# Kernel tuning notes

Hardware: AMD Instinct MI355X
Metric: run time of the kernel (lower is better)

## Reference

```python
import jax, jax.numpy as jnp
import numpy as np

LN_EPS = 1e-5


def setup_inputs() -> dict:
    key = jax.random.key(0)
    ks = jax.random.split(key, 8)
    N, H, E, D, B = 262144, 768, 768, 2048, 65536
    return {
        "u_t": jax.random.normal(ks[0], (B, E), dtype=jnp.float32),
        "s_i": jax.random.randint(ks[1], (B,), 0, N, dtype=jnp.int64),
        "speaker_embeddings": jax.random.normal(ks[2], (N, H), dtype=jnp.float32),
        "W1": jax.random.normal(ks[3], (D, H + E), dtype=jnp.float32) * 0.02,
        "b1": jax.random.normal(ks[4], (D,), dtype=jnp.float32) * 0.02,
        "W2": jax.random.normal(ks[5], (H, D), dtype=jnp.float32) * 0.02,
        "b2": jax.random.normal(ks[6], (H,), dtype=jnp.float32) * 0.02,
        "ln_gamma": jnp.ones((H,), dtype=jnp.float32),
        "ln_beta": jnp.zeros((H,), dtype=jnp.float32),
    }


def reference(u_t, s_i, speaker_embeddings, W1, b1, W2, b2, ln_gamma, ln_beta):
    # gather speaker vectors: [B, H]
    h_t = speaker_embeddings[s_i]
    # concat [u_t, h_t] along features: [B, E+H]
    x = jnp.concatenate([u_t, h_t], axis=-1)
    # Linear -> GELU (exact, torch default) -> (Dropout=identity in eval)
    h = jax.nn.gelu(jnp.einsum("bf,df->bd", x, W1) + b1, approximate=False)
    # Linear -> (Dropout=identity) : [B, H]
    y = jnp.einsum("bd,hd->bh", h, W2) + b2
    # LayerNorm over last dim
    mu = jnp.mean(y, axis=-1, keepdims=True)
    var = jnp.mean((y - mu) ** 2, axis=-1, keepdims=True)
    new_h_t = (y - mu) * jax.lax.rsqrt(var + LN_EPS) * ln_gamma + ln_beta
    # scatter-add back into the memory table (duplicates accumulate)
    updated = speaker_embeddings.at[s_i].add(new_h_t)
    return new_h_t, updated
```

## Files before the change

### kernel.cpp

```cpp
#include <hip/hip_runtime.h>
#include <hip/hip_bf16.h>

typedef unsigned short u16;
typedef unsigned int u32;
typedef short bf16x8 __attribute__((ext_vector_type(8)));
typedef float f32x4 __attribute__((ext_vector_type(4)));

#define BAR() asm volatile("s_barrier" ::: "memory")
#define WAITV8() asm volatile("s_waitcnt vmcnt(8)" ::: "memory")
#define WAITV4() asm volatile("s_waitcnt vmcnt(4)" ::: "memory")
#define WAITV0() asm volatile("s_waitcnt vmcnt(0)" ::: "memory")
#define WAITL() asm volatile("s_waitcnt lgkmcnt(0)" ::: "memory")

__device__ __forceinline__ unsigned pk2(float lo, float hi) {
    unsigned a = (unsigned)__builtin_bit_cast(u16, __float2bfloat16(lo));
    unsigned b = (unsigned)__builtin_bit_cast(u16, __float2bfloat16(hi));
    return a | (b << 16);
}
__device__ __forceinline__ u16 f2bf(float v) {
    return __builtin_bit_cast(u16, __float2bfloat16(v));
}
__device__ __forceinline__ void gl_lds16(const u16* g, u16* l) {
    __builtin_amdgcn_global_load_lds(
        (const __attribute__((address_space(1))) u32*)g,
        (__attribute__((address_space(3))) u32*)l, 16, 0, 0);
}

__global__ void cvtbf(const float4* __restrict__ s, uint2* __restrict__ d, int n4) {
    int i = blockIdx.x * blockDim.x + threadIdx.x;
    int stride = gridDim.x * blockDim.x;
    for (; i < n4; i += stride) {
        float4 f = s[i];
        uint2 o;
        o.x = pk2(f.x, f.y);
        o.y = pk2(f.z, f.w);
        d[i] = o;
    }
}

__global__ __launch_bounds__(256) void xbuild(const float* __restrict__ u_t,
                                              const float* __restrict__ emb,
                                              const int* __restrict__ s_i,
                                              u16* __restrict__ xb) {
    const long u = (long)blockIdx.x * blockDim.x + threadIdx.x;
    const int row = (int)(u / 192);
    const int c8 = (int)(u % 192);
    const float* src = (c8 < 96) ? (u_t + (long)row * 768 + c8 * 8)
                                 : (emb + (long)s_i[row] * 768 + (c8 - 96) * 8);
    float4 f0 = ((const float4*)src)[0];
    float4 f1 = ((const float4*)src)[1];
    uint4 o;
    o.x = pk2(f0.x, f0.y);
    o.y = pk2(f0.z, f0.w);
    o.z = pk2(f1.x, f1.y);
    o.w = pk2(f1.z, f1.w);
    *(uint4*)(xb + u * 8) = o;
}

template <int LDK, int NT, int TN, int EPI, int CMOD>
__global__ __launch_bounds__(512, 2) void gemm256(
    const u16* __restrict__ Ag, const u16* __restrict__ Bg,
    const float* __restrict__ bias, u16* __restrict__ outb,
    float* __restrict__ outf, const float4* __restrict__ csrc,
    float4* __restrict__ cdst, long ccount, int cstride) {
    __shared__ __align__(16) u16 lds[65536];

    const int tid = threadIdx.x;
    const int nblk = (int)gridDim.x;
    const int chunk = nblk >> 3;
    const int swz = ((int)blockIdx.x & 7) * chunk + ((int)blockIdx.x >> 3);

    if constexpr (CMOD > 0) {
        if ((swz % CMOD) == CMOD - 1) {
            long i = (long)(swz / CMOD) * 512 + tid;
            for (; i < ccount; i += cstride) cdst[i] = csrc[i];
            return;
        }
    }
    const int tile = (CMOD > 0) ? (swz - swz / CMOD) : swz;
    const int tm = tile / TN, tn = tile % TN;
    const long rowBase = (long)tm * 256;
    const long colBase = (long)tn * 256;

    const int lane = tid & 63;
    const int wv = tid >> 6;
    const int wm = wv >> 2;
    const int wn = wv & 3;

    const int srow = tid >> 2;
    const int gch = (tid & 3) ^ ((srow >> 1) & 3);
    const u16* pA = Ag + (rowBase + srow) * (long)LDK + gch * 8;
    const u16* pB = Bg + (colBase + srow) * (long)LDK + gch * 8;
    const int dstBase = wv * 512;

    auto stageA = [&](int kt, int b) {
        const u16* s = pA + kt * 32;
        u16* d = lds + b * 16384 + dstBase;
        gl_lds16(s, d);
        gl_lds16(s + (long)128 * LDK, d + 4096);
    };
    auto stageB = [&](int kt, int b) {
        const u16* s = pB + kt * 32;
        u16* d = lds + b * 16384 + 8192 + dstBase;
        gl_lds16(s, d);
        gl_lds16(s + (long)128 * LDK, d + 4096);
    };

    const int l15 = lane & 15, lc = lane >> 4;
    int offA[8], offB[4];
#pragma unroll
    for (int i = 0; i < 8; ++i) {
        int r = wm * 128 + i * 16 + l15;
        offA[i] = r * 32 + ((lc ^ ((r >> 1) & 3)) << 3);
    }
#pragma unroll
    for (int n = 0; n < 4; ++n) {
        int r = wn * 64 + n * 16 + l15;
        offB[n] = r * 32 + ((lc ^ ((r >> 1) & 3)) << 3);
    }

    f32x4 acc[8][4];
    const f32x4 zero = {0.f, 0.f, 0.f, 0.f};
#pragma unroll
    for (int m = 0; m < 8; ++m)
#pragma unroll
        for (int n = 0; n < 4; ++n) acc[m][n] = zero;

    stageA(0, 0); stageB(0, 0);
    stageA(1, 1); stageB(1, 1);
    stageA(2, 2); stageB(2, 2);
    WAITV8();
    BAR();

    bf16x8 bA[4], bB[4];
    for (int kt = 0; kt < NT; ++kt) {
        const int b = kt & 3;
        const u16* rA = lds + b * 16384;
        const u16* rB = rA + 8192;
        const bool pf = (kt + 3 < NT);

#pragma unroll
        for (int n = 0; n < 4; ++n) bB[n] = *(const bf16x8*)(rB + offB[n]);
#pragma unroll
        for (int m = 0; m < 4; ++m) bA[m] = *(const bf16x8*)(rA + offA[m]);
        if (pf) stageA(kt + 3, (kt + 3) & 3);
        BAR();
        WAITL();
        __builtin_amdgcn_s_setprio(1);
#pragma unroll
        for (int m = 0; m < 4; ++m)
#pragma unroll
            for (int n = 0; n < 4; ++n)
                acc[m][n] = __builtin_amdgcn_mfma_f32_16x16x32_bf16(bA[m], bB[n], acc[m][n], 0, 0, 0);
        __builtin_amdgcn_s_setprio(0);
        BAR();

#pragma unroll
        for (int m = 0; m < 4; ++m) bA[m] = *(const bf16x8*)(rA + offA[4 + m]);
        if (pf) stageB(kt + 3, (kt + 3) & 3);
        BAR();
        WAITL();
        __builtin_amdgcn_s_setprio(1);
#pragma unroll
        for (int m = 0; m < 4; ++m)
#pragma unroll
            for (int n = 0; n < 4; ++n)
                acc[4 + m][n] = __builtin_amdgcn_mfma_f32_16x16x32_bf16(bA[m], bB[n], acc[4 + m][n], 0, 0, 0);
        __builtin_amdgcn_s_setprio(0);
        if (pf) { WAITV8(); }
        else if (kt + 2 < NT) { WAITV4(); }
        else { WAITV0(); }
        BAR();
    }

    const int N = TN * 256;
#pragma unroll
    for (int n = 0; n < 4; ++n) {
        long gc = colBase + wn * 64 + n * 16 + l15;
        float bv = bias[gc];
#pragma unroll
        for (int i = 0; i < 8; ++i) {
            long gr = rowBase + wm * 128 + i * 16 + (lc << 2);
#pragma unroll
            for (int j = 0; j < 4; ++j) {
                float v = acc[i][n][j] + bv;
                if constexpr (EPI == 0) {
                    v = 0.5f * v * (1.0f + erff(v * 0.70710678118f));
                    outb[(gr + j) * N + gc] = f2bf(v);
                } else {
                    outf[(gr + j) * N + gc] = v;
                }
            }
        }
    }
}

__global__ __launch_bounds__(256) void ln_scatter(float* __restrict__ y,
                                                  const float* __restrict__ gamma,
                                                  const float* __restrict__ beta,
                                                  const int* __restrict__ s_i,
                                                  float* __restrict__ upd) {
    const int lane = threadIdx.x & 63;
    const long row = (long)blockIdx.x * 4 + (threadIdx.x >> 6);
    const long base = row * 768;
    float v[12];
#pragma unroll
    for (int i = 0; i < 12; ++i) v[i] = y[base + i * 64 + lane];
    float s = 0.f, q = 0.f;
#pragma unroll
    for (int i = 0; i < 12; ++i) { s += v[i]; q += v[i] * v[i]; }
#pragma unroll
    for (int off = 32; off > 0; off >>= 1) {
        s += __shfl_xor(s, off, 64);
        q += __shfl_xor(q, off, 64);
    }
    const float mu = s * (1.f / 768.f);
    const float var = q * (1.f / 768.f) - mu * mu;
    const float inv = rsqrtf(var + 1e-5f);
    const long si = s_i[row];
#pragma unroll
    for (int i = 0; i < 12; ++i) {
        int c = i * 64 + lane;
        float r = (v[i] - mu) * inv * gamma[c] + beta[c];
        y[base + c] = r;
        atomicAdd(&upd[si * 768 + c], r);
    }
}

__global__ void copy4(const float4* __restrict__ s, float4* __restrict__ d, long n) {
    long i = (long)blockIdx.x * blockDim.x + threadIdx.x;
    long stride = (long)gridDim.x * blockDim.x;
    for (; i < n; i += stride) d[i] = s[i];
}

extern "C" void kernel_launch(void* const* d_in, const int* in_sizes, int n_in,
                              void* d_out, int out_size, void* d_ws, size_t ws_size,
                              hipStream_t stream) {
    const float* u_t = (const float*)d_in[0];
    const int* s_i = (const int*)d_in[1];
    const float* emb = (const float*)d_in[2];
    const float* W1 = (const float*)d_in[3];
    const float* b1 = (const float*)d_in[4];
    const float* W2 = (const float*)d_in[5];
    const float* b2 = (const float*)d_in[6];
    const float* gamma = (const float*)d_in[7];
    const float* beta = (const float*)d_in[8];

    float* out = (float*)d_out;
    float* newh = out;
    float* upd = out + 50331648L;

    u16* base = (u16*)upd;
    u16* xb = base;
    u16* w1b = base + 100663296L;
    u16* hbuf = base + 103809024L;
    u16* w2b = base + 238026752L;

    const float4* embq = (const float4*)emb;
    float4* updq = (float4*)upd;

    cvtbf<<<1024, 256, 0, stream>>>((const float4*)W1, (uint2*)w1b, 786432);
    cvtbf<<<1024, 256, 0, stream>>>((const float4*)W2, (uint2*)w2b, 393216);
    xbuild<<<49152, 256, 0, stream>>>(u_t, emb, s_i, xb);
    gemm256<1536, 48, 8, 0, 5><<<2560, 512, 0, stream>>>(
        xb, w1b, b1, hbuf, nullptr,
        embq + 29949952L, updq + 29949952L, 20381696L, 262144);
    gemm256<2048, 64, 3, 1, 4><<<1024, 512, 0, stream>>>(
        hbuf, w2b, b2, nullptr, newh,
        embq, updq, 12976128L, 131072);
    copy4<<<2048, 256, 0, stream>>>(embq + 12976128L, updq + 12976128L, 16973824L);
    ln_scatter<<<16384, 256, 0, stream>>>(newh, gamma, beta, s_i, upd);
}
```

Measured before the change: 1.427 ms.

## Replace pipelined 256x256 GEMM with simple unpipelined 128x128 tile GEMM

Replaces the 512-thread 256x256-tile GEMM, which used a 4-stage global-to-LDS prefetch pipeline, split barriers, priority hints, and copy blocks interleaved with the embedding-table copy, with a 256-thread 128x128-tile kernel. The new kernel loads a single K=64 stage and synchronises twice per iteration, so nothing is prefetched. The embedding copy is moved entirely into a standalone copy kernel. This looks like a simplification or fallback that gives up latency hiding and reuse per tile in exchange for more blocks and simpler code.

```diff
diff --git a/kernel.cpp b/kernel.cpp
--- a/kernel.cpp
+++ b/kernel.cpp
@@ -5,12 +5,6 @@
 typedef unsigned int u32;
 typedef short bf16x8 __attribute__((ext_vector_type(8)));
 typedef float f32x4 __attribute__((ext_vector_type(4)));
-
-#define BAR() asm volatile("s_barrier" ::: "memory")
-#define WAITV8() asm volatile("s_waitcnt vmcnt(8)" ::: "memory")
-#define WAITV4() asm volatile("s_waitcnt vmcnt(4)" ::: "memory")
-#define WAITV0() asm volatile("s_waitcnt vmcnt(0)" ::: "memory")
-#define WAITL() asm volatile("s_waitcnt lgkmcnt(0)" ::: "memory")
 
 __device__ __forceinline__ unsigned pk2(float lo, float hi) {
     unsigned a = (unsigned)__builtin_bit_cast(u16, __float2bfloat16(lo));
@@ -57,133 +51,94 @@
     *(uint4*)(xb + u * 8) = o;
 }
 
-template <int LDK, int NT, int TN, int EPI, int CMOD>
-__global__ __launch_bounds__(512, 2) void gemm256(
+template <int LDK, int NT, int TN, int EPI>
+__global__ __launch_bounds__(256) void gemm128(
     const u16* __restrict__ Ag, const u16* __restrict__ Bg,
     const float* __restrict__ bias, u16* __restrict__ outb,
-    float* __restrict__ outf, const float4* __restrict__ csrc,
-    float4* __restrict__ cdst, long ccount, int cstride) {
-    __shared__ __align__(16) u16 lds[65536];
+    float* __restrict__ outf) {
+    __shared__ __align__(16) u16 As[8192];
+    __shared__ __align__(16) u16 Bs[8192];
 
     const int tid = threadIdx.x;
-    const int nblk = (int)gridDim.x;
-    const int chunk = nblk >> 3;
-    const int swz = ((int)blockIdx.x & 7) * chunk + ((int)blockIdx.x >> 3);
-
-    if constexpr (CMOD > 0) {
-        if ((swz % CMOD) == CMOD - 1) {
-            long i = (long)(swz / CMOD) * 512 + tid;
-            for (; i < ccount; i += cstride) cdst[i] = csrc[i];
-            return;
-        }
-    }
-    const int tile = (CMOD > 0) ? (swz - swz / CMOD) : swz;
+    const int lane = tid & 63;
+    const int cpx = (int)gridDim.x >> 3;
+    const int tile = ((int)blockIdx.x & 7) * cpx + ((int)blockIdx.x >> 3);
     const int tm = tile / TN, tn = tile % TN;
-    const long rowBase = (long)tm * 256;
-    const long colBase = (long)tn * 256;
-
-    const int lane = tid & 63;
+    const long rowBase = (long)tm * 128;
+    const long colBase = (long)tn * 128;
+
+    const int srow = tid >> 3;
+    const int sc = tid & 7;
+    const u16* gA[4];
+    const u16* gB[4];
+#pragma unroll
+    for (int p = 0; p < 4; ++p) {
+        int row = p * 32 + srow;
+        int gch = sc ^ (row & 7);
+        gA[p] = Ag + (rowBase + row) * (long)LDK + gch * 8;
+        gB[p] = Bg + (colBase + row) * (long)LDK + gch * 8;
+    }
+
+    auto stage = [&](int kt) {
+#pragma unroll
+        for (int p = 0; p < 4; ++p) {
+            gl_lds16(gA[p] + kt * 64, As + p * 2048 + tid * 8);
+            gl_lds16(gB[p] + kt * 64, Bs + p * 2048 + tid * 8);
+        }
+    };
+
+    const int l15 = lane & 15, lc = lane >> 4;
     const int wv = tid >> 6;
-    const int wm = wv >> 2;
-    const int wn = wv & 3;
-
-    const int srow = tid >> 2;
-    const int gch = (tid & 3) ^ ((srow >> 1) & 3);
-    const u16* pA = Ag + (rowBase + srow) * (long)LDK + gch * 8;
-    const u16* pB = Bg + (colBase + srow) * (long)LDK + gch * 8;
-    const int dstBase = wv * 512;
-
-    auto stageA = [&](int kt, int b) {
-        const u16* s = pA + kt * 32;
-        u16* d = lds + b * 16384 + dstBase;
-        gl_lds16(s, d);
-        gl_lds16(s + (long)128 * LDK, d + 4096);
-    };
-    auto stageB = [&](int kt, int b) {
-        const u16* s = pB + kt * 32;
-        u16* d = lds + b * 16384 + 8192 + dstBase;
-        gl_lds16(s, d);
-        gl_lds16(s + (long)128 * LDK, d + 4096);
-    };
-
-    const int l15 = lane & 15, lc = lane >> 4;
-    int offA[8], offB[4];
-#pragma unroll
-    for (int i = 0; i < 8; ++i) {
-        int r = wm * 128 + i * 16 + l15;
-        offA[i] = r * 32 + ((lc ^ ((r >> 1) & 3)) << 3);
-    }
+    const int wr = wv >> 1, wc = wv & 1;
+    int offA[2][4], offB[2][4];
+#pragma unroll
+    for (int kk = 0; kk < 2; ++kk) {
+#pragma unroll
+        for (int m = 0; m < 4; ++m) {
+            int r = wr * 64 + m * 16 + l15;
+            offA[kk][m] = r * 64 + ((((kk * 4 + lc)) ^ (r & 7)) << 3);
+            int c = wc * 64 + m * 16 + l15;
+            offB[kk][m] = c * 64 + ((((kk * 4 + lc)) ^ (c & 7)) << 3);
+        }
+    }
+
+    f32x4 acc[4][4];
+    const f32x4 zero = {0.f, 0.f, 0.f, 0.f};
+#pragma unroll
+    for (int m = 0; m < 4; ++m)
+#pragma unroll
+        for (int n = 0; n < 4; ++n) acc[m][n] = zero;
+
+    for (int kt = 0; kt < NT; ++kt) {
+        stage(kt);
+        __syncthreads();
+#pragma unroll
+        for (int kk = 0; kk < 2; ++kk) {
+            bf16x8 a[4], b[4];
+#pragma unroll
+            for (int m = 0; m < 4; ++m) a[m] = *(const bf16x8*)(As + offA[kk][m]);
+#pragma unroll
+            for (int n = 0; n < 4; ++n) b[n] = *(const bf16x8*)(Bs + offB[kk][n]);
+#pragma unroll
+            for (int m = 0; m < 4; ++m)
+#pragma unroll
+                for (int n = 0; n < 4; ++n)
+                    acc[m][n] = __builtin_amdgcn_mfma_f32_16x16x32_bf16(a[m], b[n], acc[m][n], 0, 0, 0);
+        }
+        __syncthreads();
+    }
+
+    const int N = TN * 128;
 #pragma unroll
     for (int n = 0; n < 4; ++n) {
-        int r = wn * 64 + n * 16 + l15;
-        offB[n] = r * 32 + ((lc ^ ((r >> 1) & 3)) << 3);
-    }
-
-    f32x4 acc[8][4];
-    const f32x4 zero = {0.f, 0.f, 0.f, 0.f};
-#pragma unroll
-    for (int m = 0; m < 8; ++m)
-#pragma unroll
-        for (int n = 0; n < 4; ++n) acc[m][n] = zero;
-
-    stageA(0, 0); stageB(0, 0);
-    stageA(1, 1); stageB(1, 1);
-    stageA(2, 2); stageB(2, 2);
-    WAITV8();
-    BAR();
-
-    bf16x8 bA[4], bB[4];
-    for (int kt = 0; kt < NT; ++kt) {
-        const int b = kt & 3;
-        const u16* rA = lds + b * 16384;
-        const u16* rB = rA + 8192;
-        const bool pf = (kt + 3 < NT);
-
-#pragma unroll
-        for (int n = 0; n < 4; ++n) bB[n] = *(const bf16x8*)(rB + offB[n]);
-#pragma unroll
-        for (int m = 0; m < 4; ++m) bA[m] = *(const bf16x8*)(rA + offA[m]);
-        if (pf) stageA(kt + 3, (kt + 3) & 3);
-        BAR();
-        WAITL();
-        __builtin_amdgcn_s_setprio(1);
-#pragma unroll
-        for (int m = 0; m < 4; ++m)
-#pragma unroll
-            for (int n = 0; n < 4; ++n)
-                acc[m][n] = __builtin_amdgcn_mfma_f32_16x16x32_bf16(bA[m], bB[n], acc[m][n], 0, 0, 0);
-        __builtin_amdgcn_s_setprio(0);
-        BAR();
-
-#pragma unroll
-        for (int m = 0; m < 4; ++m) bA[m] = *(const bf16x8*)(rA + offA[4 + m]);
-        if (pf) stageB(kt + 3, (kt + 3) & 3);
-        BAR();
-        WAITL();
-        __builtin_amdgcn_s_setprio(1);
-#pragma unroll
-        for (int m = 0; m < 4; ++m)
-#pragma unroll
-            for (int n = 0; n < 4; ++n)
-                acc[4 + m][n] = __builtin_amdgcn_mfma_f32_16x16x32_bf16(bA[m], bB[n], acc[4 + m][n], 0, 0, 0);
-        __builtin_amdgcn_s_setprio(0);
-        if (pf) { WAITV8(); }
-        else if (kt + 2 < NT) { WAITV4(); }
-        else { WAITV0(); }
-        BAR();
-    }
-
-    const int N = TN * 256;
-#pragma unroll
-    for (int n = 0; n < 4; ++n) {
-        long gc = colBase + wn * 64 + n * 16 + l15;
+        long gc = colBase + wc * 64 + n * 16 + l15;
         float bv = bias[gc];
 #pragma unroll
-        for (int i = 0; i < 8; ++i) {
-            long gr = rowBase + wm * 128 + i * 16 + (lc << 2);
+        for (int m = 0; m < 4; ++m) {
+            long gr = rowBase + wr * 64 + m * 16 + (lc << 2);
 #pragma unroll
             for (int j = 0; j < 4; ++j) {
-                float v = acc[i][n][j] + bv;
+                float v = acc[m][n][j] + bv;
                 if constexpr (EPI == 0) {
                     v = 0.5f * v * (1.0f + erff(v * 0.70710678118f));
                     outb[(gr + j) * N + gc] = f2bf(v);
@@ -256,18 +211,11 @@
     u16* hbuf = base + 103809024L;
     u16* w2b = base + 238026752L;
 
-    const float4* embq = (const float4*)emb;
-    float4* updq = (float4*)upd;
-
     cvtbf<<<1024, 256, 0, stream>>>((const float4*)W1, (uint2*)w1b, 786432);
     cvtbf<<<1024, 256, 0, stream>>>((const float4*)W2, (uint2*)w2b, 393216);
     xbuild<<<49152, 256, 0, stream>>>(u_t, emb, s_i, xb);
-    gemm256<1536, 48, 8, 0, 5><<<2560, 512, 0, stream>>>(
-        xb, w1b, b1, hbuf, nullptr,
-        embq + 29949952L, updq + 29949952L, 20381696L, 262144);
-    gemm256<2048, 64, 3, 1, 4><<<1024, 512, 0, stream>>>(
-        hbuf, w2b, b2, nullptr, newh,
-        embq, updq, 12976128L, 131072);
-    copy4<<<2048, 256, 0, stream>>>(embq + 12976128L, updq + 12976128L, 16973824L);
+    gemm128<1536, 24, 16, 0><<<8192, 256, 0, stream>>>(xb, w1b, b1, hbuf, nullptr);
+    gemm128<2048, 32, 6, 1><<<3072, 256, 0, stream>>>(hbuf, w2b, b2, nullptr, newh);
+    copy4<<<2048, 256, 0, stream>>>((const float4*)emb, (float4*)upd, 50331648L);
     ln_scatter<<<16384, 256, 0, stream>>>(newh, gamma, beta, s_i, upd);
 }
```

Result: slower. 1.529 ms (+7.2%).
